# Kernel tuning notes

Hardware: AMD Instinct MI355X
Metric: run time of the kernel (lower is better)

Reference implementation:

```python
import jax, jax.numpy as jnp
import numpy as np

B, T, D, H = 4, 2048, 1024, 16
HD = D // H


def setup_inputs() -> dict:
    key = jax.random.key(0)
    kq, kk, kv, k1, k2, k3, k4 = jax.random.split(key, 7)
    q = jax.random.normal(kq, (B, T, D), dtype=jnp.float32)
    k = jax.random.normal(kk, (B, T, D), dtype=jnp.float32)
    v = jax.random.normal(kv, (B, T, D), dtype=jnp.float32)
    # causal mask, broadcast over heads: [B, 1, T, T]
    mask = jnp.broadcast_to(jnp.tril(jnp.ones((T, T), dtype=bool)), (B, 1, T, T))
    s = 0.02
    Wq = jax.random.normal(k1, (D, D), dtype=jnp.float32) * s
    Wk = jax.random.normal(k2, (D, D), dtype=jnp.float32) * s
    Wv = jax.random.normal(k3, (D, D), dtype=jnp.float32) * s
    Wo = jax.random.normal(k4, (D, D), dtype=jnp.float32) * s
    return {"q": q, "k": k, "v": v, "mask": mask,
            "Wq": Wq, "Wk": Wk, "Wv": Wv, "Wo": Wo}


def reference(q, k, v, mask, Wq, Wk, Wv, Wo):
    scale = HD ** -0.5
    # nn.Linear: y = x @ W.T  (bias=False)
    qh = (q @ Wq.T).reshape(B, T, H, HD).transpose(0, 2, 1, 3)  # [B,H,T,HD]
    kh = (k @ Wk.T).reshape(B, -1, H, HD).transpose(0, 2, 1, 3)
    vh = (v @ Wv.T).reshape(B, -1, H, HD).transpose(0, 2, 1, 3)
    scores = jnp.einsum('bhqd,bhkd->bhqk', qh, kh) * scale  # [B,H,T,T]
    # dropout p=0.0 -> identity (applied pre-mask in original)
    scores = jnp.where(mask, scores, -jnp.inf)
    probs = jax.nn.softmax(scores, axis=-1)
    attn = jnp.einsum('bhqk,bhkd->bhqd', probs, vh)  # [B,H,T,HD]
    attn = attn.transpose(0, 2, 1, 3).reshape(B, T, D)
    return attn @ Wo.T
```

## Files before the change

### kernel.cpp

```cpp
#include <hip/hip_runtime.h>
#include <stdint.h>

#define B_  4
#define T_  2048
#define D_  1024
#define H_  16
#define HD_ 64

typedef __bf16 bf16_t;
typedef __bf16 bf16x8 __attribute__((ext_vector_type(8)));
typedef float  f32x4  __attribute__((ext_vector_type(4)));
typedef float  f32x16 __attribute__((ext_vector_type(16)));

__device__ __forceinline__ uint16_t f2bf(float f) {
  uint32_t x = __float_as_uint(f);
  uint32_t r = (x + 0x7fffu + ((x >> 16) & 1u)) >> 16;
  return (uint16_t)r;
}

__device__ __forceinline__ uint32_t pack2(float a, float b) {
  return (uint32_t)f2bf(a) | ((uint32_t)f2bf(b) << 16);
}

__device__ __forceinline__ float exp2a(float x) {
  float r;
  asm("v_exp_f32 %0, %1" : "=v"(r) : "v"(x));
  return r;
}

__device__ __forceinline__ uint32_t cvtpk(float a, float b) {
  uint32_t r;
  asm("v_cvt_pk_bf16_f32 %0, %1, %2" : "=v"(r) : "v"(a), "v"(b));
  return r;
}

__device__ __forceinline__ void plswap(uint32_t& a, uint32_t& b) {
  asm("v_permlane32_swap_b32 %0, %1" : "+v"(a), "+v"(b));
}

__device__ __forceinline__ void gll16(const void* g, void* l) {
  __builtin_amdgcn_global_load_lds(
      (const __attribute__((address_space(1))) void*)g,
      (__attribute__((address_space(3))) void*)l, 16, 0, 0);
}

__global__ __launch_bounds__(256) void cvt_bf16(const float* __restrict__ in,
                                                uint16_t* __restrict__ out, int n) {
  int i = (blockIdx.x * 256 + threadIdx.x) * 8;
  if (i >= n) return;
  float4 a = *(const float4*)(in + i);
  float4 b = *(const float4*)(in + i + 4);
  uint4 u;
  u.x = pack2(a.x, a.y);
  u.y = pack2(a.z, a.w);
  u.z = pack2(b.x, b.y);
  u.w = pack2(b.z, b.w);
  *(uint4*)(out + i) = u;
}

template <int MODE>
__global__ __launch_bounds__(256, 2)
void gemm_bt(const uint16_t* __restrict__ A, const uint16_t* __restrict__ W,
             void* __restrict__ Out, int K, float scale) {
  __shared__ __align__(16) uint16_t As[128 * 64];
  __shared__ __align__(16) uint16_t Bs[128 * 64];
  const int tid = threadIdx.x;
  const int wid = tid >> 6, lane = tid & 63;
  const int fr = lane & 15, fq = lane >> 4;
  const int wr = wid >> 1, wc = wid & 1;
  const int m0 = blockIdx.x * 128, n0 = blockIdx.y * 128;
  const int srow = lane >> 3, c8 = lane & 7;

  f32x4 acc[4][4];
#pragma unroll
  for (int i = 0; i < 4; ++i)
#pragma unroll
    for (int j = 0; j < 4; ++j) acc[i][j] = (f32x4){0.f, 0.f, 0.f, 0.f};

  for (int k0 = 0; k0 < K; k0 += 64) {
#pragma unroll
    for (int c = 0; c < 4; ++c) {
      int slot = wid * 4 + c;
      int row = slot * 8 + srow;
      int sw = (c8 ^ (row & 7)) << 3;
      gll16(A + (size_t)(m0 + row) * K + k0 + sw, &As[slot * 512]);
      gll16(W + (size_t)(n0 + row) * K + k0 + sw, &Bs[slot * 512]);
    }
    __syncthreads();
#pragma unroll
    for (int ks = 0; ks < 2; ++ks) {
      bf16x8 af[4], bfr[4];
#pragma unroll
      for (int mf = 0; mf < 4; ++mf) {
        int r = wr * 64 + mf * 16 + fr;
        int ch = (fq + ks * 4) ^ (r & 7);
        af[mf] = *(const bf16x8*)&As[r * 64 + ch * 8];
      }
#pragma unroll
      for (int nf = 0; nf < 4; ++nf) {
        int r = wc * 64 + nf * 16 + fr;
        int ch = (fq + ks * 4) ^ (r & 7);
        bfr[nf] = *(const bf16x8*)&Bs[r * 64 + ch * 8];
      }
#pragma unroll
      for (int mf = 0; mf < 4; ++mf)
#pragma unroll
        for (int nf = 0; nf < 4; ++nf)
          acc[mf][nf] = __builtin_amdgcn_mfma_f32_16x16x32_bf16(af[mf], bfr[nf],
                                                                acc[mf][nf], 0, 0, 0);
    }
    __syncthreads();
  }

#pragma unroll
  for (int mf = 0; mf < 4; ++mf) {
#pragma unroll
    for (int nf = 0; nf < 4; ++nf) {
      if (MODE == 2) {
        int m = m0 + wr * 64 + mf * 16 + fq * 4;
        int n = n0 + wc * 64 + nf * 16 + fr;
        int b = m >> 11, t = m & (T_ - 1);
        int h = n >> 6, hd = n & 63;
        uint2 pk;
        pk.x = pack2(acc[mf][nf][0], acc[mf][nf][1]);
        pk.y = pack2(acc[mf][nf][2], acc[mf][nf][3]);
        uint16_t* dst = (uint16_t*)Out +
                        ((((size_t)b * H_ + h) * HD_ + hd) * T_ + t);
        *(uint2*)dst = pk;
      } else {
#pragma unroll
        for (int r = 0; r < 4; ++r) {
          int m = m0 + wr * 64 + mf * 16 + fq * 4 + r;
          int n = n0 + wc * 64 + nf * 16 + fr;
          float v = acc[mf][nf][r] * scale;
          if (MODE == 3) {
            ((float*)Out)[(size_t)m * D_ + n] = v;
          } else {
            int b = m >> 11, t = m & (T_ - 1);
            int h = n >> 6, hd = n & 63;
            ((uint16_t*)Out)[((((size_t)b * H_ + h) * T_ + t) << 6) + hd] = f2bf(v);
          }
        }
      }
    }
  }
}

__global__ __launch_bounds__(512)
void attn_fwd(const uint16_t* __restrict__ Qh, const uint16_t* __restrict__ Kh,
              const uint16_t* __restrict__ Vt, uint16_t* __restrict__ O) {
  __shared__ __align__(16) uint16_t SB[4][64 * 64];

  const int tid = threadIdx.x, wid = tid >> 6, lane = tid & 63;
  const int ql = lane & 31, hi = lane >> 5;
  const int bid = blockIdx.x;
  const int qb = (T_ / 256 - 1) - (bid >> 6);
  const int bh = bid & 63;
  const int q0 = qb * 256;
  const int wq0 = q0 + wid * 32;
  const size_t hoff = (size_t)bh * T_ * HD_;
  const uint16_t* Qp = Qh + hoff;
  const uint16_t* Kp = Kh + hoff;
  const uint16_t* Vp = Vt + hoff;

  bf16x8 qf[4];
  {
    const uint16_t* qrow = Qp + (size_t)(wq0 + ql) * 64 + hi * 8;
#pragma unroll
    for (int ks = 0; ks < 4; ++ks) qf[ks] = *(const bf16x8*)(qrow + ks * 16);
  }

  float m = -1e30f, l = 0.f;
  f32x16 acc[2];
#pragma unroll
  for (int mo = 0; mo < 2; ++mo)
#pragma unroll
    for (int r = 0; r < 16; ++r) acc[mo][r] = 0.f;

  const int ntiles = 4 * qb + 4;

#define STAGE(buf, t)                                                        \
  do {                                                                       \
    int row = wid * 8 + (lane >> 3);                                         \
    int sw = ((lane & 7) ^ (row & 7)) << 3;                                  \
    gll16(Kp + (size_t)((t) * 64 + row) * 64 + sw, &SB[buf][wid * 512]);     \
    gll16(Vp + (size_t)row * T_ + (t) * 64 + sw, &SB[2 + (buf)][wid * 512]); \
  } while (0)

  STAGE(0, 0);
  asm volatile("s_waitcnt vmcnt(0)" ::: "memory");
  __builtin_amdgcn_s_barrier();

  for (int it = 0; it < ntiles; ++it) {
    const int cur = it & 1;
    if (it + 1 < ntiles) STAGE(cur ^ 1, it + 1);

    if (it * 64 <= wq0 + 31) {
      f32x16 st[2];
#pragma unroll
      for (int mm = 0; mm < 2; ++mm)
#pragma unroll
        for (int r = 0; r < 16; ++r) st[mm][r] = 0.f;
#pragma unroll
      for (int ks = 0; ks < 4; ++ks) {
#pragma unroll
        for (int mm = 0; mm < 2; ++mm) {
          int row = mm * 32 + ql;
          int ch = (ks * 2 + hi) ^ (row & 7);
          bf16x8 kf = *(const bf16x8*)&SB[cur][row * 64 + ch * 8];
          st[mm] = __builtin_amdgcn_mfma_f32_32x32x16_bf16(kf, qf[ks], st[mm], 0, 0, 0);
        }
      }

      if (it * 64 + 63 > wq0) {
        int qg = wq0 + ql;
#pragma unroll
        for (int mm = 0; mm < 2; ++mm)
#pragma unroll
          for (int r = 0; r < 16; ++r) {
            int kv = it * 64 + mm * 32 + (r & 3) + 8 * (r >> 2) + 4 * hi;
            if (kv > qg) st[mm][r] = -1e30f;
          }
      }

      float pm = st[0][0];
#pragma unroll
      for (int r = 1; r < 16; ++r) pm = fmaxf(pm, st[0][r]);
#pragma unroll
      for (int r = 0; r < 16; ++r) pm = fmaxf(pm, st[1][r]);
      pm = fmaxf(pm, __shfl_xor(pm, 32));

      if (__any(pm > m + 8.f)) {
        float mn = fmaxf(m, pm);
        float sf = exp2a(m - mn);
        m = mn;
        l *= sf;
#pragma unroll
        for (int mo = 0; mo < 2; ++mo)
#pragma unroll
          for (int r = 0; r < 16; ++r) acc[mo][r] *= sf;
      }

      float rs = 0.f;
#pragma unroll
      for (int mm = 0; mm < 2; ++mm)
#pragma unroll
        for (int r = 0; r < 16; ++r) {
          float p = exp2a(st[mm][r] - m);
          st[mm][r] = p;
          rs += p;
        }
      rs += __shfl_xor(rs, 32);
      l += rs;

      bf16x8 pf[4];
#pragma unroll
      for (int mm = 0; mm < 2; ++mm)
#pragma unroll
        for (int g = 0; g < 2; ++g) {
          uint32_t a1 = cvtpk(st[mm][8 * g + 0], st[mm][8 * g + 1]);
          uint32_t a2 = cvtpk(st[mm][8 * g + 2], st[mm][8 * g + 3]);
          uint32_t b1 = cvtpk(st[mm][8 * g + 4], st[mm][8 * g + 5]);
          uint32_t b2 = cvtpk(st[mm][8 * g + 6], st[mm][8 * g + 7]);
          plswap(a1, b1);
          plswap(a2, b2);
          union { uint32_t w[4]; bf16x8 v; } u;
          u.w[0] = a1; u.w[1] = a2; u.w[2] = b1; u.w[3] = b2;
          pf[mm * 2 + g] = u.v;
        }

#pragma unroll
      for (int ks = 0; ks < 4; ++ks) {
#pragma unroll
        for (int mo = 0; mo < 2; ++mo) {
          int row = mo * 32 + ql;
          int ch = (ks * 2 + hi) ^ (row & 7);
          bf16x8 vf = *(const bf16x8*)&SB[2 + cur][row * 64 + ch * 8];
          acc[mo] = __builtin_amdgcn_mfma_f32_32x32x16_bf16(vf, pf[ks], acc[mo], 0, 0, 0);
        }
      }
    }

    asm volatile("s_waitcnt vmcnt(0)" ::: "memory");
    __builtin_amdgcn_s_barrier();
  }
#undef STAGE

  __syncthreads();
  uint16_t* ost = &SB[0][0];
  {
    float inv = 1.0f / l;
    uint16_t* wst = ost + wid * 2048;
#pragma unroll
    for (int mo = 0; mo < 2; ++mo)
#pragma unroll
      for (int r = 0; r < 16; r += 2) {
        int hd = mo * 32 + (r & 3) + 8 * (r >> 2) + 4 * hi;
        uint32_t pk = pack2(acc[mo][r] * inv, acc[mo][r + 1] * inv);
        int col = hd ^ ((ql & 7) << 3);
        *(uint32_t*)&wst[ql * 64 + col] = pk;
      }
  }
  __syncthreads();
  {
    int row = tid >> 1, half = tid & 1;
    int r7 = row & 7;
    int b = bh >> 4, h = bh & 15;
    size_t g = (size_t)(b * T_ + q0 + row) * D_ + h * 64 + half * 32;
#pragma unroll
    for (int j = 0; j < 4; ++j) {
      int cc = half * 4 + j;
      uint4 val = *(const uint4*)&ost[row * 64 + (cc ^ r7) * 8];
      *(uint4*)&O[g + j * 8] = val;
    }
  }
}

extern "C" void kernel_launch(void* const* d_in, const int* in_sizes, int n_in,
                              void* d_out, int out_size, void* d_ws, size_t ws_size,
                              hipStream_t stream) {
  (void)in_sizes; (void)n_in; (void)out_size; (void)ws_size;
  const float* q  = (const float*)d_in[0];
  const float* k  = (const float*)d_in[1];
  const float* v  = (const float*)d_in[2];
  const float* Wq = (const float*)d_in[4];
  const float* Wk = (const float*)d_in[5];
  const float* Wv = (const float*)d_in[6];
  const float* Wo = (const float*)d_in[7];

  uint8_t* ws = (uint8_t*)d_ws;
  const size_t MB = 1u << 20;
  uint16_t* WQB = (uint16_t*)(ws + 0 * MB);
  uint16_t* WKB = (uint16_t*)(ws + 2 * MB);
  uint16_t* WVB = (uint16_t*)(ws + 4 * MB);
  uint16_t* WOB = (uint16_t*)(ws + 6 * MB);
  uint16_t* XQ  = (uint16_t*)(ws + 8 * MB);
  uint16_t* XK  = (uint16_t*)(ws + 24 * MB);
  uint16_t* XV  = (uint16_t*)(ws + 40 * MB);
  uint16_t* QH  = (uint16_t*)(ws + 56 * MB);
  uint16_t* KH  = (uint16_t*)(ws + 72 * MB);
  uint16_t* VT  = (uint16_t*)(ws + 88 * MB);
  uint16_t* AC  = (uint16_t*)(ws + 8 * MB);

  const int nBig = B_ * T_ * D_;
  const int nW   = D_ * D_;
  cvt_bf16<<<nBig / 2048, 256, 0, stream>>>(q, XQ, nBig);
  cvt_bf16<<<nBig / 2048, 256, 0, stream>>>(k, XK, nBig);
  cvt_bf16<<<nBig / 2048, 256, 0, stream>>>(v, XV, nBig);
  cvt_bf16<<<nW / 2048, 256, 0, stream>>>(Wq, WQB, nW);
  cvt_bf16<<<nW / 2048, 256, 0, stream>>>(Wk, WKB, nW);
  cvt_bf16<<<nW / 2048, 256, 0, stream>>>(Wv, WVB, nW);
  cvt_bf16<<<nW / 2048, 256, 0, stream>>>(Wo, WOB, nW);

  dim3 ggrid(B_ * T_ / 128, D_ / 128);
  const float qscale = 0.125f * 1.44269504088896340736f;
  gemm_bt<0><<<ggrid, 256, 0, stream>>>(XQ, WQB, QH, D_, qscale);
  gemm_bt<1><<<ggrid, 256, 0, stream>>>(XK, WKB, KH, D_, 1.0f);
  gemm_bt<2><<<ggrid, 256, 0, stream>>>(XV, WVB, VT, D_, 1.0f);

  attn_fwd<<<dim3(T_ / 256 * 64), 512, 0, stream>>>(QH, KH, VT, AC);

  gemm_bt<3><<<ggrid, 256, 0, stream>>>(AC, WOB, d_out, D_, 1.0f);
}
```

Baseline: 186.4 us.

## Batch conversions and QKV GEMMs, add 4-stage pipelined 128x256 GEMM kernel

Merges the seven bf16 conversion launches into two batched launches. Replaces the synchronous 128x128 GEMM with a 512-thread 128x256-tile kernel that uses a 4-buffer global_load_lds pipeline with vmcnt-based waits, setprio around the MFMAs, and a grouped block-swizzle for L2 locality. The Q/K/V projections run as one 768-block launch, and the output projection reuses the same kernel. This is meant to hide global load latency and cut launch overhead, in exchange for more LDS per block and more complex synchronisation.

Result: faster. 175.7 us (-5.7%).

```diff
diff --git a/kernel.cpp b/kernel.cpp
--- a/kernel.cpp
+++ b/kernel.cpp
@@ -6,6 +6,7 @@
 #define D_  1024
 #define H_  16
 #define HD_ 64
+#define KK_ 1024
 
 typedef __bf16 bf16_t;
 typedef __bf16 bf16x8 __attribute__((ext_vector_type(8)));
@@ -44,10 +45,15 @@
       (__attribute__((address_space(3))) void*)l, 16, 0, 0);
 }
 
-__global__ __launch_bounds__(256) void cvt_bf16(const float* __restrict__ in,
-                                                uint16_t* __restrict__ out, int n) {
+__global__ __launch_bounds__(256) void cvt3(const float* __restrict__ s0,
+                                            const float* __restrict__ s1,
+                                            const float* __restrict__ s2,
+                                            uint16_t* __restrict__ d0,
+                                            uint16_t* __restrict__ d1,
+                                            uint16_t* __restrict__ d2) {
+  const float* in = blockIdx.y == 0 ? s0 : (blockIdx.y == 1 ? s1 : s2);
+  uint16_t* out = blockIdx.y == 0 ? d0 : (blockIdx.y == 1 ? d1 : d2);
   int i = (blockIdx.x * 256 + threadIdx.x) * 8;
-  if (i >= n) return;
   float4 a = *(const float4*)(in + i);
   float4 b = *(const float4*)(in + i + 4);
   uint4 u;
@@ -58,18 +64,57 @@
   *(uint4*)(out + i) = u;
 }
 
-template <int MODE>
-__global__ __launch_bounds__(256, 2)
-void gemm_bt(const uint16_t* __restrict__ A, const uint16_t* __restrict__ W,
-             void* __restrict__ Out, int K, float scale) {
-  __shared__ __align__(16) uint16_t As[128 * 64];
-  __shared__ __align__(16) uint16_t Bs[128 * 64];
+__global__ __launch_bounds__(256) void cvtW(const float* __restrict__ s0,
+                                            const float* __restrict__ s1,
+                                            const float* __restrict__ s2,
+                                            const float* __restrict__ s3,
+                                            uint16_t* __restrict__ d0,
+                                            uint16_t* __restrict__ d1,
+                                            uint16_t* __restrict__ d2,
+                                            uint16_t* __restrict__ d3) {
+  const float* in = blockIdx.y == 0 ? s0 : (blockIdx.y == 1 ? s1 :
+                    (blockIdx.y == 2 ? s2 : s3));
+  uint16_t* out = blockIdx.y == 0 ? d0 : (blockIdx.y == 1 ? d1 :
+                  (blockIdx.y == 2 ? d2 : d3));
+  int i = (blockIdx.x * 256 + threadIdx.x) * 8;
+  float4 a = *(const float4*)(in + i);
+  float4 b = *(const float4*)(in + i + 4);
+  uint4 u;
+  u.x = pack2(a.x, a.y);
+  u.y = pack2(a.z, a.w);
+  u.z = pack2(b.x, b.y);
+  u.w = pack2(b.z, b.w);
+  *(uint4*)(out + i) = u;
+}
+
+__global__ __launch_bounds__(512, 2)
+void gemm8(const uint16_t* __restrict__ a0, const uint16_t* __restrict__ a1,
+           const uint16_t* __restrict__ a2, const uint16_t* __restrict__ w0,
+           const uint16_t* __restrict__ w1, const uint16_t* __restrict__ w2,
+           void* __restrict__ o0, void* __restrict__ o1, void* __restrict__ o2,
+           int mode_base, float scale0) {
+  __shared__ __align__(16) uint16_t Ab[4][128 * 32];
+  __shared__ __align__(16) uint16_t Bb[4][256 * 32];
+
+  const int nwg = gridDim.x;
+  const int bid = blockIdx.x;
+  const int cpx = nwg >> 3;
+  const int swz = (bid & 7) * cpx + (bid >> 3);
+  const int g = swz >> 8;
+  const int r = swz & 255;
+  const int mt = r >> 2, nt = r & 3;
+  const int m0 = mt * 128, n0 = nt * 256;
+
+  const uint16_t* A = g == 0 ? a0 : (g == 1 ? a1 : a2);
+  const uint16_t* W = g == 0 ? w0 : (g == 1 ? w1 : w2);
+  void* Out = g == 0 ? o0 : (g == 1 ? o1 : o2);
+  const int mode = mode_base + g;
+  const float scale = (mode == 0) ? scale0 : 1.0f;
+
   const int tid = threadIdx.x;
   const int wid = tid >> 6, lane = tid & 63;
   const int fr = lane & 15, fq = lane >> 4;
-  const int wr = wid >> 1, wc = wid & 1;
-  const int m0 = blockIdx.x * 128, n0 = blockIdx.y * 128;
-  const int srow = lane >> 3, c8 = lane & 7;
+  const int wm = wid >> 2, wn = wid & 3;
 
   f32x4 acc[4][4];
 #pragma unroll
@@ -77,69 +122,90 @@
 #pragma unroll
     for (int j = 0; j < 4; ++j) acc[i][j] = (f32x4){0.f, 0.f, 0.f, 0.f};
 
-  for (int k0 = 0; k0 < K; k0 += 64) {
-#pragma unroll
-    for (int c = 0; c < 4; ++c) {
-      int slot = wid * 4 + c;
-      int row = slot * 8 + srow;
-      int sw = (c8 ^ (row & 7)) << 3;
-      gll16(A + (size_t)(m0 + row) * K + k0 + sw, &As[slot * 512]);
-      gll16(W + (size_t)(n0 + row) * K + k0 + sw, &Bs[slot * 512]);
+  const int NT = KK_ / 32;
+
+#define STAGE(bi, t)                                                          \
+  do {                                                                        \
+    {                                                                         \
+      int row = wid * 16 + (lane >> 2);                                       \
+      int ch = (lane & 3) ^ ((row >> 1) & 3);                                 \
+      gll16(A + (size_t)(m0 + row) * KK_ + (t) * 32 + ch * 8,                 \
+            &Ab[bi][wid * 512]);                                              \
+    }                                                                         \
+    _Pragma("unroll")                                                         \
+    for (int c = 0; c < 2; ++c) {                                             \
+      int row = c * 128 + wid * 16 + (lane >> 2);                             \
+      int ch = (lane & 3) ^ ((row >> 1) & 3);                                 \
+      gll16(W + (size_t)(n0 + row) * KK_ + (t) * 32 + ch * 8,                 \
+            &Bb[bi][c * 4096 + wid * 512]);                                   \
+    }                                                                         \
+  } while (0)
+
+  STAGE(0, 0);
+  STAGE(1, 1);
+  STAGE(2, 2);
+  asm volatile("s_waitcnt vmcnt(6)" ::: "memory");
+  __builtin_amdgcn_s_barrier();
+
+#pragma unroll 4
+  for (int t = 0; t < NT; ++t) {
+    const int cur = t & 3;
+    bf16x8 af[4], bfr[4];
+#pragma unroll
+    for (int i = 0; i < 4; ++i) {
+      int ra = wm * 64 + i * 16 + fr;
+      af[i] = *(const bf16x8*)&Ab[cur][ra * 32 + ((fq ^ ((ra >> 1) & 3)) << 3)];
+      int rb = wn * 64 + i * 16 + fr;
+      bfr[i] = *(const bf16x8*)&Bb[cur][rb * 32 + ((fq ^ ((rb >> 1) & 3)) << 3)];
     }
-    __syncthreads();
-#pragma unroll
-    for (int ks = 0; ks < 2; ++ks) {
-      bf16x8 af[4], bfr[4];
-#pragma unroll
-      for (int mf = 0; mf < 4; ++mf) {
-        int r = wr * 64 + mf * 16 + fr;
-        int ch = (fq + ks * 4) ^ (r & 7);
-        af[mf] = *(const bf16x8*)&As[r * 64 + ch * 8];
-      }
-#pragma unroll
-      for (int nf = 0; nf < 4; ++nf) {
-        int r = wc * 64 + nf * 16 + fr;
-        int ch = (fq + ks * 4) ^ (r & 7);
-        bfr[nf] = *(const bf16x8*)&Bs[r * 64 + ch * 8];
-      }
-#pragma unroll
-      for (int mf = 0; mf < 4; ++mf)
-#pragma unroll
-        for (int nf = 0; nf < 4; ++nf)
-          acc[mf][nf] = __builtin_amdgcn_mfma_f32_16x16x32_bf16(af[mf], bfr[nf],
-                                                                acc[mf][nf], 0, 0, 0);
+    if (t + 3 < NT) STAGE((t + 3) & 3, t + 3);
+    __builtin_amdgcn_s_setprio(1);
+#pragma unroll
+    for (int mf = 0; mf < 4; ++mf)
+#pragma unroll
+      for (int nf = 0; nf < 4; ++nf)
+        acc[mf][nf] = __builtin_amdgcn_mfma_f32_16x16x32_bf16(af[mf], bfr[nf],
+                                                              acc[mf][nf], 0, 0, 0);
+    __builtin_amdgcn_s_setprio(0);
+    if (t + 1 < NT) {
+      if (t + 3 < NT) {
+        asm volatile("s_waitcnt vmcnt(6)" ::: "memory");
+      } else if (t + 2 < NT) {
+        asm volatile("s_waitcnt vmcnt(3)" ::: "memory");
+      } else {
+        asm volatile("s_waitcnt vmcnt(0)" ::: "memory");
+      }
+      __builtin_amdgcn_s_barrier();
     }
-    __syncthreads();
-  }
+  }
+#undef STAGE
 
 #pragma unroll
   for (int mf = 0; mf < 4; ++mf) {
 #pragma unroll
     for (int nf = 0; nf < 4; ++nf) {
-      if (MODE == 2) {
-        int m = m0 + wr * 64 + mf * 16 + fq * 4;
-        int n = n0 + wc * 64 + nf * 16 + fr;
+      int m = m0 + wm * 64 + mf * 16 + fq * 4;
+      int n = n0 + wn * 64 + nf * 16 + fr;
+      if (mode == 2) {
         int b = m >> 11, t = m & (T_ - 1);
         int h = n >> 6, hd = n & 63;
         uint2 pk;
         pk.x = pack2(acc[mf][nf][0], acc[mf][nf][1]);
         pk.y = pack2(acc[mf][nf][2], acc[mf][nf][3]);
-        uint16_t* dst = (uint16_t*)Out +
-                        ((((size_t)b * H_ + h) * HD_ + hd) * T_ + t);
+        uint16_t* dst = (uint16_t*)Out + ((((size_t)b * H_ + h) * HD_ + hd) * T_ + t);
         *(uint2*)dst = pk;
+      } else if (mode == 3) {
+#pragma unroll
+        for (int rr = 0; rr < 4; ++rr)
+          ((float*)Out)[(size_t)(m + rr) * D_ + n] = acc[mf][nf][rr];
       } else {
 #pragma unroll
-        for (int r = 0; r < 4; ++r) {
-          int m = m0 + wr * 64 + mf * 16 + fq * 4 + r;
-          int n = n0 + wc * 64 + nf * 16 + fr;
-          float v = acc[mf][nf][r] * scale;
-          if (MODE == 3) {
-            ((float*)Out)[(size_t)m * D_ + n] = v;
-          } else {
-            int b = m >> 11, t = m & (T_ - 1);
-            int h = n >> 6, hd = n & 63;
-            ((uint16_t*)Out)[((((size_t)b * H_ + h) * T_ + t) << 6) + hd] = f2bf(v);
-          }
+        for (int rr = 0; rr < 4; ++rr) {
+          int mm = m + rr;
+          int b = mm >> 11, t = mm & (T_ - 1);
+          int h = n >> 6, hd = n & 63;
+          ((uint16_t*)Out)[((((size_t)b * H_ + h) * T_ + t) << 6) + hd] =
+              f2bf(acc[mf][nf][rr] * scale);
         }
       }
     }
@@ -342,23 +408,16 @@
   uint16_t* VT  = (uint16_t*)(ws + 88 * MB);
   uint16_t* AC  = (uint16_t*)(ws + 8 * MB);
 
-  const int nBig = B_ * T_ * D_;
-  const int nW   = D_ * D_;
-  cvt_bf16<<<nBig / 2048, 256, 0, stream>>>(q, XQ, nBig);
-  cvt_bf16<<<nBig / 2048, 256, 0, stream>>>(k, XK, nBig);
-  cvt_bf16<<<nBig / 2048, 256, 0, stream>>>(v, XV, nBig);
-  cvt_bf16<<<nW / 2048, 256, 0, stream>>>(Wq, WQB, nW);
-  cvt_bf16<<<nW / 2048, 256, 0, stream>>>(Wk, WKB, nW);
-  cvt_bf16<<<nW / 2048, 256, 0, stream>>>(Wv, WVB, nW);
-  cvt_bf16<<<nW / 2048, 256, 0, stream>>>(Wo, WOB, nW);
-
-  dim3 ggrid(B_ * T_ / 128, D_ / 128);
+  cvt3<<<dim3(B_ * T_ * D_ / 2048, 3), 256, 0, stream>>>(q, k, v, XQ, XK, XV);
+  cvtW<<<dim3(D_ * D_ / 2048, 4), 256, 0, stream>>>(Wq, Wk, Wv, Wo, WQB, WKB, WVB, WOB);
+
   const float qscale = 0.125f * 1.44269504088896340736f;
-  gemm_bt<0><<<ggrid, 256, 0, stream>>>(XQ, WQB, QH, D_, qscale);
-  gemm_bt<1><<<ggrid, 256, 0, stream>>>(XK, WKB, KH, D_, 1.0f);
-  gemm_bt<2><<<ggrid, 256, 0, stream>>>(XV, WVB, VT, D_, 1.0f);
+
+  gemm8<<<dim3(768), 512, 0, stream>>>(XQ, XK, XV, WQB, WKB, WVB,
+                                       QH, KH, VT, 0, qscale);
 
   attn_fwd<<<dim3(T_ / 256 * 64), 512, 0, stream>>>(QH, KH, VT, AC);
 
-  gemm_bt<3><<<ggrid, 256, 0, stream>>>(AC, WOB, d_out, D_, 1.0f);
-}
+  gemm8<<<dim3(256), 512, 0, stream>>>(AC, nullptr, nullptr, WOB, nullptr, nullptr,
+                                       d_out, nullptr, nullptr, 3, 1.0f);
+}
```
